# Kernel tuning notes

Measured on AMD Instinct MI355X. Metric: run time of the kernel, lower is better.

## Reference

```python
import jax, jax.numpy as jnp
import numpy as np

NUM_HEADS = 8
PW_GROUPS = 3 * NUM_HEADS  # grouped 1x1 conv groups


def _conv(x, w, groups):
    # x: [B, Cin, H, W], w: [Cout, Cin/groups, kh, kw]
    return jax.lax.conv_general_dilated(
        x, w, window_strides=(1, 1), padding='SAME',
        feature_group_count=groups,
        dimension_numbers=('NCHW', 'OIHW', 'NCHW'))


def setup_inputs() -> dict:
    key = jax.random.key(0)
    ks = jax.random.split(key, 12)
    dim, N, B = 512, 4096, 2
    C = dim // 2  # 256
    s = 0.02
    return {
        'x': jax.random.normal(ks[0], (B, N, dim), jnp.float32),
        'w_reduce': jax.random.normal(ks[1], (dim, C), jnp.float32) * s,
        'w_qkv': jax.random.normal(ks[2], (C, 3 * C), jnp.float32) * s,
        'dw0': jax.random.normal(ks[3], (3 * C, 1, 3, 3), jnp.float32) * s,
        'pw0': jax.random.normal(ks[4], (3 * C, 3 * C // PW_GROUPS, 1, 1), jnp.float32) * s,
        'dw1': jax.random.normal(ks[5], (3 * C, 1, 5, 5), jnp.float32) * s,
        'pw1': jax.random.normal(ks[6], (3 * C, 3 * C // PW_GROUPS, 1, 1), jnp.float32) * s,
        'dw2': jax.random.normal(ks[7], (3 * C, 1, 7, 7), jnp.float32) * s,
        'pw2': jax.random.normal(ks[8], (3 * C, 3 * C // PW_GROUPS, 1, 1), jnp.float32) * s,
        'w_reduce2': jax.random.normal(ks[9], (6 * dim, 3 * C), jnp.float32) * s,
        'w_proj': jax.random.normal(ks[10], (C, dim), jnp.float32) * s,
        'b_proj': jax.random.normal(ks[11], (dim,), jnp.float32) * s,
    }


def reference(x, w_reduce, w_qkv, dw0, pw0, dw1, pw1, dw2, pw2,
              w_reduce2, w_proj, b_proj):
    B, N, dim = x.shape
    Hn = NUM_HEADS
    x = x @ w_reduce                       # [B, N, C]
    C = x.shape[-1]
    hd = C // Hn
    scale = hd ** -0.5
    Hs = int(np.sqrt(N))                   # spatial side

    qkv = x @ w_qkv                        # [B, N, 3C]
    qkv_img = qkv.transpose(0, 2, 1).reshape(B, 3 * C, Hs, Hs)

    branches = [qkv_img]
    for dw, pw in ((dw0, pw0), (dw1, pw1), (dw2, pw2)):
        y = _conv(qkv_img, dw, groups=3 * C)      # depthwise
        y = _conv(y, pw, groups=PW_GROUPS)        # grouped 1x1
        branches.append(y)
    cat = jnp.concatenate(branches, axis=1)       # [B, 12C, Hs, Hs]
    cat = cat.reshape(B, 12 * C, N).transpose(0, 2, 1)  # [B, N, 6*dim]
    msq = cat @ w_reduce2                          # [B, N, 3C]

    qkv = msq.reshape(B, N, 3, Hn, hd).transpose(2, 0, 3, 1, 4)  # [3,B,H,N,hd]
    q, k, v = qkv[0], qkv[1], qkv[2]

    # chunked attention: 2 chunks of N//2 tokens, attention within each chunk
    Nc = N // 2
    qc = q.reshape(B, Hn, 2, Nc, hd)
    kc = k.reshape(B, Hn, 2, Nc, hd)
    vc = v.reshape(B, Hn, 2, Nc, hd)
    attn = jnp.einsum('bhcqd,bhckd->bhcqk', qc, kc) * scale
    attn = jax.nn.softmax(attn, axis=-1)
    out = jnp.einsum('bhcqk,bhckd->bhcqd', attn, vc)  # [B,H,2,Nc,hd]
    out = out.transpose(0, 2, 3, 1, 4).reshape(B, N, C)
    return out @ w_proj + b_proj                  # [B, N, dim]
```

## Files before the change

kernel.cpp:

```cpp
#include <hip/hip_runtime.h>
#include <hip/hip_bf16.h>

typedef __bf16 bf16x8 __attribute__((ext_vector_type(8)));
typedef __bf16 bf16x4v __attribute__((ext_vector_type(4)));
typedef float f32x4 __attribute__((ext_vector_type(4)));
typedef unsigned int u32x4 __attribute__((ext_vector_type(4)));

using bf16 = __hip_bfloat16;

__global__ __launch_bounds__(256) void k_cvt_bf16(const float* __restrict__ in,
                                                  bf16* __restrict__ out) {
  const int i = (blockIdx.x * 256 + threadIdx.x) * 4;
  float4 v = *reinterpret_cast<const float4*>(in + i);
  out[i + 0] = __float2bfloat16(v.x);
  out[i + 1] = __float2bfloat16(v.y);
  out[i + 2] = __float2bfloat16(v.z);
  out[i + 3] = __float2bfloat16(v.w);
}

__global__ __launch_bounds__(256) void k_transpose_bf16(const float* __restrict__ w,
                                                        bf16* __restrict__ wt,
                                                        int K, int N) {
  __shared__ float t[32][33];
  const int k0 = blockIdx.x * 32, n0 = blockIdx.y * 32;
  const int tx = threadIdx.x & 31, ty = threadIdx.x >> 5;
#pragma unroll
  for (int i = 0; i < 32; i += 8)
    t[ty + i][tx] = w[(size_t)(k0 + ty + i) * N + n0 + tx];
  __syncthreads();
#pragma unroll
  for (int i = 0; i < 32; i += 8)
    wt[(size_t)(n0 + ty + i) * K + k0 + tx] = __float2bfloat16(t[tx][ty + i]);
}

__global__ __launch_bounds__(256) void k_transpose2d(const bf16* __restrict__ in,
                                                     bf16* __restrict__ out,
                                                     int R, int C) {
  __shared__ unsigned short tl[64][65];
  const int c0 = blockIdx.x * 64, r0 = blockIdx.y * 64;
  const size_t zb = (size_t)blockIdx.z * R * C;
  const int tx = threadIdx.x & 63, ty = threadIdx.x >> 6;
  const unsigned short* ip = (const unsigned short*)in + zb;
  unsigned short* op = (unsigned short*)out + zb;
#pragma unroll
  for (int i = 0; i < 64; i += 4)
    tl[ty + i][tx] = ip[(size_t)(r0 + ty + i) * C + c0 + tx];
  __syncthreads();
#pragma unroll
  for (int i = 0; i < 64; i += 4)
    op[(size_t)(c0 + ty + i) * R + r0 + tx] = tl[tx][ty + i];
}

__global__ __launch_bounds__(256) void k_gemm_bt(
    const bf16* __restrict__ A0, const bf16* __restrict__ A1,
    const bf16* __restrict__ A2, const bf16* __restrict__ A3,
    const bf16* __restrict__ Bt, bf16* __restrict__ Cb,
    float* __restrict__ Cf, const float* __restrict__ bias,
    int N, int K, int srcK, int split_bk) {
  __shared__ __align__(16) bf16 As[2][128 * 64];
  __shared__ __align__(16) bf16 Bs[2][128 * 64];
  const int tid = threadIdx.x;
  const int lane = tid & 63;
  const int wv = tid >> 6;
  const size_t M0 = (size_t)blockIdx.x * 128;
  const int N0 = blockIdx.y * 128;
  const int wr = (wv >> 1) * 64, wc = (wv & 1) * 64;
  const int fr = lane & 15, fo = (lane >> 4) * 8;
  const int lrow = lane >> 3, lcol = (lane & 7) << 3;
  f32x4 acc[4][4] = {};

  auto stage = [&](int kt, int buf) {
    const int s = kt / split_bk;
    const bf16* __restrict__ Ak = (s == 0) ? A0 : (s == 1) ? A1 : (s == 2) ? A2 : A3;
    const size_t aofs = (size_t)(kt - s * split_bk) * 64;
    const size_t bofs = (size_t)kt * 64;
#pragma unroll
    for (int ld = 0; ld < 4; ++ld) {
      const int row = wv * 32 + ld * 8 + lrow;
      const bf16* ga = Ak + (M0 + row) * (size_t)srcK + aofs + lcol;
      __builtin_amdgcn_global_load_lds(
          (const __attribute__((address_space(1))) unsigned int*)ga,
          (__attribute__((address_space(3))) unsigned int*)(As[buf] + (wv * 32 + ld * 8) * 64),
          16, 0, 0);
      const bf16* gb = Bt + (size_t)(N0 + row) * K + bofs + lcol;
      __builtin_amdgcn_global_load_lds(
          (const __attribute__((address_space(1))) unsigned int*)gb,
          (__attribute__((address_space(3))) unsigned int*)(Bs[buf] + (wv * 32 + ld * 8) * 64),
          16, 0, 0);
    }
  };

  const int nsteps = K >> 6;
  stage(0, 0);
  __syncthreads();
  int cur = 0;
  for (int kt = 0; kt < nsteps; ++kt) {
    if (kt + 1 < nsteps) stage(kt + 1, cur ^ 1);
#pragma unroll
    for (int kk = 0; kk < 64; kk += 32) {
      bf16x8 a[4], b[4];
#pragma unroll
      for (int m = 0; m < 4; ++m)
        a[m] = *reinterpret_cast<const bf16x8*>(As[cur] + (wr + m * 16 + fr) * 64 + kk + fo);
#pragma unroll
      for (int n = 0; n < 4; ++n)
        b[n] = *reinterpret_cast<const bf16x8*>(Bs[cur] + (wc + n * 16 + fr) * 64 + kk + fo);
#pragma unroll
      for (int m = 0; m < 4; ++m)
#pragma unroll
        for (int n = 0; n < 4; ++n)
          acc[m][n] = __builtin_amdgcn_mfma_f32_16x16x32_bf16(a[m], b[n], acc[m][n], 0, 0, 0);
    }
    __syncthreads();
    cur ^= 1;
  }

  const int rb = (lane >> 4) * 4;
#pragma unroll
  for (int m = 0; m < 4; ++m) {
#pragma unroll
    for (int n = 0; n < 4; ++n) {
      const size_t row = M0 + wr + m * 16 + rb;
      const int col = N0 + wc + n * 16 + fr;
      if (Cb != nullptr) {
#pragma unroll
        for (int r = 0; r < 4; ++r)
          Cb[(row + r) * N + col] = __float2bfloat16(acc[m][n][r]);
      } else {
        const float bb = bias[col];
#pragma unroll
        for (int r = 0; r < 4; ++r)
          Cf[(row + r) * N + col] = acc[m][n][r] + bb;
      }
    }
  }
}

template <int KS>
__global__ __launch_bounds__(256) void k_dwconv_img(const bf16* __restrict__ in,
                                                    const float* __restrict__ w,
                                                    bf16* __restrict__ out) {
  constexpr int P = KS / 2;
  constexpr int ROWS = 64 + 2 * P;
  constexpr int PITCH = 80;
  constexpr int NCHUNK = ROWS * PITCH * 2 / 16;
  __shared__ __align__(16) bf16 pl[ROWS * PITCH];
  const int t = threadIdx.x;
  const int c = blockIdx.x, b = blockIdx.y;
  const bf16* __restrict__ ip = in + ((size_t)b * 768 + c) * 4096;
  bf16* __restrict__ op = out + ((size_t)b * 768 + c) * 4096;

  u32x4* pl4 = reinterpret_cast<u32x4*>(pl);
  for (int i = t; i < NCHUNK; i += 256) pl4[i] = u32x4{0, 0, 0, 0};
  __syncthreads();
  for (int q = t; q < 512; q += 256) {
    const int px0 = q * 8;
    const int y = px0 >> 6, x = px0 & 63;
    u32x4 v = *reinterpret_cast<const u32x4*>(ip + px0);
    *reinterpret_cast<u32x4*>(&pl[(y + P) * PITCH + 8 + x]) = v;
  }
  __syncthreads();

  float wk[KS * KS];
#pragma unroll
  for (int i = 0; i < KS * KS; ++i) wk[i] = w[c * KS * KS + i];

  const int x = t & 63;
  const int y0 = (t >> 6) * 16;
  float win[KS][KS];
#pragma unroll
  for (int r = 0; r < 2 * P; ++r)
#pragma unroll
    for (int kx = 0; kx < KS; ++kx)
      win[r % KS][kx] = __bfloat162float(pl[(y0 + r) * PITCH + 8 + x - P + kx]);
#pragma unroll
  for (int yy = 0; yy < 16; ++yy) {
    constexpr int twoP = 2 * P;
#pragma unroll
    for (int kx = 0; kx < KS; ++kx)
      win[(yy + twoP) % KS][kx] =
          __bfloat162float(pl[(y0 + yy + twoP) * PITCH + 8 + x - P + kx]);
    float acc = 0.f;
#pragma unroll
    for (int ky = 0; ky < KS; ++ky)
#pragma unroll
      for (int kx = 0; kx < KS; ++kx)
        acc += win[(yy + ky) % KS][kx] * wk[ky * KS + kx];
    op[(y0 + yy) * 64 + x] = __float2bfloat16(acc);
  }
}

__global__ __launch_bounds__(256) void k_pwconv_img(const bf16* __restrict__ in,
                                                    const float* __restrict__ w,
                                                    bf16* __restrict__ out) {
  const int co0 = blockIdx.x * 4;
  const int g = co0 >> 5;
  const int b = blockIdx.z;
  const int px = blockIdx.y * 2048 + threadIdx.x * 8;
  const bf16* __restrict__ ip = in + ((size_t)b * 768 + g * 32) * 4096 + px;
  float acc[4][8] = {};
#pragma unroll
  for (int ci = 0; ci < 32; ++ci) {
    const bf16x8 v = *reinterpret_cast<const bf16x8*>(ip + (size_t)ci * 4096);
    float fv[8];
#pragma unroll
    for (int j = 0; j < 8; ++j) fv[j] = (float)v[j];
#pragma unroll
    for (int q = 0; q < 4; ++q) {
      const float wq = w[(co0 + q) * 32 + ci];
#pragma unroll
      for (int j = 0; j < 8; ++j) acc[q][j] += wq * fv[j];
    }
  }
#pragma unroll
  for (int q = 0; q < 4; ++q) {
    bf16x8 o;
#pragma unroll
    for (int j = 0; j < 8; ++j) o[j] = (__bf16)acc[q][j];
    *reinterpret_cast<bf16x8*>(out + ((size_t)b * 768 + co0 + q) * 4096 + px) = o;
  }
}

__global__ __launch_bounds__(256) void k_attn(const bf16* __restrict__ msq,
                                              bf16* __restrict__ out) {
  const int qt = blockIdx.x;
  const int combo = blockIdx.y;
  const int b = combo >> 4;
  const int h = (combo >> 1) & 7;
  const int ck = combo & 1;
  const int tid = threadIdx.x, lane = tid & 63, wv = tid >> 6;
  const int fr = lane & 15, hi = lane >> 4, fo = hi * 8;
  const size_t base = (size_t)b * 4096 * 768;
  const int n0 = ck * 2048 + qt * 128;

  __shared__ __align__(16) bf16 Kl[2][64][40];
  __shared__ __align__(16) bf16 Vt[2][32][72];
  __shared__ __align__(16) bf16 Pl[4][2][16][72];

  const float scale = 0.17677669529663687f;
  bf16x8 qf[2];
#pragma unroll
  for (int t = 0; t < 2; ++t) {
    const int qrow = n0 + t * 64 + wv * 16 + fr;
    const bf16x8 v =
        *reinterpret_cast<const bf16x8*>(msq + base + (size_t)qrow * 768 + h * 32 + fo);
#pragma unroll
    for (int j = 0; j < 8; ++j) qf[t][j] = (__bf16)((float)v[j] * scale);
  }

  f32x4 oacc[2][2] = {};
  float mrun[2] = {-1e30f, -1e30f};
  float lrun[2] = {0.f, 0.f};
  const int sr = tid >> 2, sdc = (tid & 3) << 3;

  u32x4 kr, vr;
  auto gload = [&](int kt) {
    const size_t rbase = base + (size_t)(ck * 2048 + kt * 64 + sr) * 768 + h * 32;
    kr = *reinterpret_cast<const u32x4*>(msq + rbase + 256 + sdc);
    vr = *reinterpret_cast<const u32x4*>(msq + rbase + 512 + sdc);
  };
  auto lwrite = [&](int buf) {
    *reinterpret_cast<u32x4*>(&Kl[buf][sr][sdc]) = kr;
    const bf16* vp = reinterpret_cast<const bf16*>(&vr);
#pragma unroll
    for (int j = 0; j < 8; ++j) Vt[buf][sdc + j][sr] = vp[j];
  };

  gload(0);
  lwrite(0);
  int cur = 0;
  for (int kt = 0; kt < 32; ++kt) {
    __syncthreads();
    if (kt + 1 < 32) gload(kt + 1);

    bf16x8 kf[4];
#pragma unroll
    for (int j = 0; j < 4; ++j)
      kf[j] = *reinterpret_cast<const bf16x8*>(&Kl[cur][j * 16 + fr][fo]);

#pragma unroll
    for (int t = 0; t < 2; ++t) {
      f32x4 sacc[4];
#pragma unroll
      for (int j = 0; j < 4; ++j) {
        const f32x4 z = {0.f, 0.f, 0.f, 0.f};
        sacc[j] = __builtin_amdgcn_mfma_f32_16x16x32_bf16(kf[j], qf[t], z, 0, 0, 0);
      }
      float mx = -1e30f;
#pragma unroll
      for (int j = 0; j < 4; ++j)
#pragma unroll
        for (int r = 0; r < 4; ++r) mx = fmaxf(mx, sacc[j][r]);
      mx = fmaxf(mx, __shfl_xor(mx, 16));
      mx = fmaxf(mx, __shfl_xor(mx, 32));
      const float mnew = fmaxf(mrun[t], mx);
      const float corr = __expf(mrun[t] - mnew);
      mrun[t] = mnew;
      float sm = 0.f;
#pragma unroll
      for (int j = 0; j < 4; ++j) {
        bf16x4v pk;
#pragma unroll
        for (int r = 0; r < 4; ++r) {
          const float pz = __expf(sacc[j][r] - mnew);
          sm += pz;
          pk[r] = (__bf16)pz;
        }
        *reinterpret_cast<bf16x4v*>(&Pl[wv][t][fr][j * 16 + hi * 4]) = pk;
      }
      sm += __shfl_xor(sm, 16);
      sm += __shfl_xor(sm, 32);
      lrun[t] = lrun[t] * corr + sm;
#pragma unroll
      for (int r = 0; r < 4; ++r) {
        const float cf = __shfl(corr, hi * 4 + r);
        oacc[t][0][r] *= cf;
        oacc[t][1][r] *= cf;
      }
    }

#pragma unroll
    for (int t = 0; t < 2; ++t)
#pragma unroll
      for (int kk = 0; kk < 2; ++kk) {
        const bf16x8 pa = *reinterpret_cast<const bf16x8*>(&Pl[wv][t][fr][kk * 32 + fo]);
#pragma unroll
        for (int nb = 0; nb < 2; ++nb) {
          const bf16x8 vb =
              *reinterpret_cast<const bf16x8*>(&Vt[cur][nb * 16 + fr][kk * 32 + fo]);
          oacc[t][nb] = __builtin_amdgcn_mfma_f32_16x16x32_bf16(pa, vb, oacc[t][nb], 0, 0, 0);
        }
      }

    if (kt + 1 < 32) lwrite(cur ^ 1);
    cur ^= 1;
  }

#pragma unroll
  for (int t = 0; t < 2; ++t)
#pragma unroll
    for (int r = 0; r < 4; ++r) {
      const float lf = __shfl(lrun[t], hi * 4 + r);
      const float inv = 1.f / lf;
      const int row = n0 + t * 64 + wv * 16 + hi * 4 + r;
#pragma unroll
      for (int nb = 0; nb < 2; ++nb)
        out[((size_t)b * 4096 + row) * 256 + h * 32 + nb * 16 + fr] =
            __float2bfloat16(oacc[t][nb][r] * inv);
    }
}

extern "C" void kernel_launch(void* const* d_in, const int* in_sizes, int n_in,
                              void* d_out, int out_size, void* d_ws, size_t ws_size,
                              hipStream_t stream) {
  (void)in_sizes; (void)n_in; (void)out_size; (void)ws_size;
  const float* x    = (const float*)d_in[0];
  const float* wrd  = (const float*)d_in[1];
  const float* wqkv = (const float*)d_in[2];
  const float* dw0  = (const float*)d_in[3];
  const float* pw0  = (const float*)d_in[4];
  const float* dw1  = (const float*)d_in[5];
  const float* pw1  = (const float*)d_in[6];
  const float* dw2  = (const float*)d_in[7];
  const float* pw2  = (const float*)d_in[8];
  const float* wrd2 = (const float*)d_in[9];
  const float* wprj = (const float*)d_in[10];
  const float* bprj = (const float*)d_in[11];
  float* out = (float*)d_out;

  char* p = (char*)d_ws;
  auto nxt = [&](size_t bytes) {
    char* r = p;
    p += (bytes + 255) & ~(size_t)255;
    return (bf16*)r;
  };
  bf16* xb   = nxt(8192ull * 512 * 2);
  bf16* xr   = nxt(8192ull * 256 * 2);
  bf16* qkvT = xb;
  bf16* wrT  = nxt(256ull * 512 * 2);
  bf16* wqT  = nxt(768ull * 256 * 2);
  bf16* wr2T = nxt(768ull * 3072 * 2);
  bf16* wpT  = nxt(512ull * 256 * 2);
  bf16* qkv  = nxt(8192ull * 768 * 2);
  bf16* dtmp = nxt(8192ull * 768 * 2);
  bf16* y0   = nxt(8192ull * 768 * 2);
  bf16* y1   = nxt(8192ull * 768 * 2);
  bf16* y2   = nxt(8192ull * 768 * 2);
  bf16* msq  = nxt(8192ull * 768 * 2);
  bf16* pwT  = msq;
  bf16* ao   = nxt(8192ull * 256 * 2);

  k_cvt_bf16<<<(8192 * 512 / 4) / 256, 256, 0, stream>>>(x, xb);
  k_transpose_bf16<<<dim3(512 / 32, 256 / 32), 256, 0, stream>>>(wrd, wrT, 512, 256);
  k_transpose_bf16<<<dim3(256 / 32, 768 / 32), 256, 0, stream>>>(wqkv, wqT, 256, 768);
  k_transpose_bf16<<<dim3(3072 / 32, 768 / 32), 256, 0, stream>>>(wrd2, wr2T, 3072, 768);
  k_transpose_bf16<<<dim3(256 / 32, 512 / 32), 256, 0, stream>>>(wprj, wpT, 256, 512);

  k_gemm_bt<<<dim3(64, 2), 256, 0, stream>>>(xb, xb, xb, xb, wrT, xr, nullptr, nullptr,
                                             256, 512, 512, 1 << 20);
  k_gemm_bt<<<dim3(64, 6), 256, 0, stream>>>(xr, xr, xr, xr, wqT, qkv, nullptr, nullptr,
                                             768, 256, 256, 1 << 20);

  k_transpose2d<<<dim3(12, 64, 2), 256, 0, stream>>>(qkv, qkvT, 4096, 768);

  k_dwconv_img<3><<<dim3(768, 2), 256, 0, stream>>>(qkvT, dw0, dtmp);
  k_pwconv_img<<<dim3(192, 2, 2), 256, 0, stream>>>(dtmp, pw0, pwT);
  k_transpose2d<<<dim3(64, 12, 2), 256, 0, stream>>>(pwT, y0, 768, 4096);

  k_dwconv_img<5><<<dim3(768, 2), 256, 0, stream>>>(qkvT, dw1, dtmp);
  k_pwconv_img<<<dim3(192, 2, 2), 256, 0, stream>>>(dtmp, pw1, pwT);
  k_transpose2d<<<dim3(64, 12, 2), 256, 0, stream>>>(pwT, y1, 768, 4096);

  k_dwconv_img<7><<<dim3(768, 2), 256, 0, stream>>>(qkvT, dw2, dtmp);
  k_pwconv_img<<<dim3(192, 2, 2), 256, 0, stream>>>(dtmp, pw2, pwT);
  k_transpose2d<<<dim3(64, 12, 2), 256, 0, stream>>>(pwT, y2, 768, 4096);

  k_gemm_bt<<<dim3(64, 6), 256, 0, stream>>>(qkv, y0, y1, y2, wr2T, msq, nullptr, nullptr,
                                             768, 3072, 768, 12);

  k_attn<<<dim3(16, 32), 256, 0, stream>>>(msq, ao);

  k_gemm_bt<<<dim3(64, 4), 256, 0, stream>>>(ao, ao, ao, ao, wpT, nullptr, out, bprj,
                                             512, 256, 256, 1 << 20);
}
```

Measured before the change: 375.2 us.

## Fold linear weights algebraically, drop pwconv kernels, retile attention with lazy rescale

Precomputes w_reduce@w_qkv into one fused weight so two GEMMs become one. Folds each grouped 1x1 pointwise conv into the corresponding rows of w_reduce2, which removes three pwconv kernels and their intermediate traffic. The attention kernel now handles 64 queries per block with twice as many blocks, skips the online-softmax rescale unless the running max grows by more than a threshold, and XOR-swizzles the V tile in shared memory to cut bank conflicts. Weight folding rounds the combined products to bf16 and changes accumulation order, so numerics shift slightly.

```diff
diff --git a/kernel.cpp b/kernel.cpp
--- a/kernel.cpp
+++ b/kernel.cpp
@@ -31,6 +31,55 @@
 #pragma unroll
   for (int i = 0; i < 32; i += 8)
     wt[(size_t)(n0 + ty + i) * K + k0 + tx] = __float2bfloat16(t[tx][ty + i]);
+}
+
+__global__ __launch_bounds__(256) void k_fuse_w12(const float* __restrict__ wrd,
+                                                  const float* __restrict__ wqkv,
+                                                  bf16* __restrict__ w12T) {
+  const int n = blockIdx.x * 64 + (threadIdx.x & 63);
+  const int k0 = blockIdx.y * 64 + (threadIdx.x >> 6) * 16;
+  float acc[16] = {};
+  for (int j = 0; j < 256; ++j) {
+    const float wq = wqkv[(size_t)j * 768 + n];
+#pragma unroll
+    for (int e = 0; e < 16; ++e) acc[e] += wrd[(size_t)(k0 + e) * 256 + j] * wq;
+  }
+  bf16x8 o0, o1;
+#pragma unroll
+  for (int e = 0; e < 8; ++e) { o0[e] = (__bf16)acc[e]; o1[e] = (__bf16)acc[8 + e]; }
+  *reinterpret_cast<bf16x8*>(w12T + (size_t)n * 512 + k0) = o0;
+  *reinterpret_cast<bf16x8*>(w12T + (size_t)n * 512 + k0 + 8) = o1;
+}
+
+__global__ __launch_bounds__(256) void k_fuse_pw(const float* __restrict__ pw0,
+                                                 const float* __restrict__ pw1,
+                                                 const float* __restrict__ pw2,
+                                                 const float* __restrict__ w2,
+                                                 bf16* __restrict__ wr2T) {
+  const int g = blockIdx.x;
+  const int n0 = blockIdx.y * 64;
+  const int i = blockIdx.z;
+  const float* __restrict__ pw = (i == 0) ? pw0 : (i == 1) ? pw1 : pw2;
+  __shared__ float pwL[32][36];
+  {
+    const int q = threadIdx.x >> 3, c4 = (threadIdx.x & 7) * 4;
+    float4 v = *reinterpret_cast<const float4*>(pw + (size_t)(g * 32 + q) * 32 + c4);
+    *reinterpret_cast<float4*>(&pwL[q][c4]) = v;
+  }
+  __syncthreads();
+  const int n = n0 + (threadIdx.x & 63);
+  const int ch = threadIdx.x >> 6;
+  const int kbase = 768 * (i + 1) + g * 32;
+  float acc[8] = {};
+  for (int q = 0; q < 32; ++q) {
+    const float w2v = w2[(size_t)(kbase + q) * 768 + n];
+#pragma unroll
+    for (int e = 0; e < 8; ++e) acc[e] += pwL[q][ch * 8 + e] * w2v;
+  }
+  bf16x8 o;
+#pragma unroll
+  for (int e = 0; e < 8; ++e) o[e] = (__bf16)acc[e];
+  *reinterpret_cast<bf16x8*>(wr2T + (size_t)n * 3072 + kbase + ch * 8) = o;
 }
 
 __global__ __launch_bounds__(256) void k_transpose2d(const bf16* __restrict__ in,
@@ -190,37 +239,6 @@
   }
 }
 
-__global__ __launch_bounds__(256) void k_pwconv_img(const bf16* __restrict__ in,
-                                                    const float* __restrict__ w,
-                                                    bf16* __restrict__ out) {
-  const int co0 = blockIdx.x * 4;
-  const int g = co0 >> 5;
-  const int b = blockIdx.z;
-  const int px = blockIdx.y * 2048 + threadIdx.x * 8;
-  const bf16* __restrict__ ip = in + ((size_t)b * 768 + g * 32) * 4096 + px;
-  float acc[4][8] = {};
-#pragma unroll
-  for (int ci = 0; ci < 32; ++ci) {
-    const bf16x8 v = *reinterpret_cast<const bf16x8*>(ip + (size_t)ci * 4096);
-    float fv[8];
-#pragma unroll
-    for (int j = 0; j < 8; ++j) fv[j] = (float)v[j];
-#pragma unroll
-    for (int q = 0; q < 4; ++q) {
-      const float wq = w[(co0 + q) * 32 + ci];
-#pragma unroll
-      for (int j = 0; j < 8; ++j) acc[q][j] += wq * fv[j];
-    }
-  }
-#pragma unroll
-  for (int q = 0; q < 4; ++q) {
-    bf16x8 o;
-#pragma unroll
-    for (int j = 0; j < 8; ++j) o[j] = (__bf16)acc[q][j];
-    *reinterpret_cast<bf16x8*>(out + ((size_t)b * 768 + co0 + q) * 4096 + px) = o;
-  }
-}
-
 __global__ __launch_bounds__(256) void k_attn(const bf16* __restrict__ msq,
                                               bf16* __restrict__ out) {
   const int qt = blockIdx.x;
@@ -231,27 +249,26 @@
   const int tid = threadIdx.x, lane = tid & 63, wv = tid >> 6;
   const int fr = lane & 15, hi = lane >> 4, fo = hi * 8;
   const size_t base = (size_t)b * 4096 * 768;
-  const int n0 = ck * 2048 + qt * 128;
+  const int n0 = ck * 2048 + qt * 64;
 
   __shared__ __align__(16) bf16 Kl[2][64][40];
   __shared__ __align__(16) bf16 Vt[2][32][72];
-  __shared__ __align__(16) bf16 Pl[4][2][16][72];
+  __shared__ __align__(16) bf16 Pl[4][16][72];
 
   const float scale = 0.17677669529663687f;
-  bf16x8 qf[2];
-#pragma unroll
-  for (int t = 0; t < 2; ++t) {
-    const int qrow = n0 + t * 64 + wv * 16 + fr;
+  bf16x8 qf;
+  {
+    const int qrow = n0 + wv * 16 + fr;
     const bf16x8 v =
         *reinterpret_cast<const bf16x8*>(msq + base + (size_t)qrow * 768 + h * 32 + fo);
 #pragma unroll
-    for (int j = 0; j < 8; ++j) qf[t][j] = (__bf16)((float)v[j] * scale);
-  }
-
-  f32x4 oacc[2][2] = {};
-  float mrun[2] = {-1e30f, -1e30f};
-  float lrun[2] = {0.f, 0.f};
+    for (int j = 0; j < 8; ++j) qf[j] = (__bf16)((float)v[j] * scale);
+  }
+
+  f32x4 oacc[2] = {};
+  float mrun = 0.f, lrun = 0.f;
   const int sr = tid >> 2, sdc = (tid & 3) << 3;
+  const int vswz = (tid & 3) << 4;
 
   u32x4 kr, vr;
   auto gload = [&](int kt) {
@@ -263,7 +280,7 @@
     *reinterpret_cast<u32x4*>(&Kl[buf][sr][sdc]) = kr;
     const bf16* vp = reinterpret_cast<const bf16*>(&vr);
 #pragma unroll
-    for (int j = 0; j < 8; ++j) Vt[buf][sdc + j][sr] = vp[j];
+    for (int j = 0; j < 8; ++j) Vt[buf][sdc + j][sr ^ vswz] = vp[j];
   };
 
   gload(0);
@@ -273,81 +290,74 @@
     __syncthreads();
     if (kt + 1 < 32) gload(kt + 1);
 
-    bf16x8 kf[4];
+    f32x4 sacc[4];
+#pragma unroll
+    for (int j = 0; j < 4; ++j) {
+      const bf16x8 kf = *reinterpret_cast<const bf16x8*>(&Kl[cur][j * 16 + fr][fo]);
+      const f32x4 z = {0.f, 0.f, 0.f, 0.f};
+      sacc[j] = __builtin_amdgcn_mfma_f32_16x16x32_bf16(kf, qf, z, 0, 0, 0);
+    }
+    float mx = -1e30f;
 #pragma unroll
     for (int j = 0; j < 4; ++j)
-      kf[j] = *reinterpret_cast<const bf16x8*>(&Kl[cur][j * 16 + fr][fo]);
-
-#pragma unroll
-    for (int t = 0; t < 2; ++t) {
-      f32x4 sacc[4];
-#pragma unroll
-      for (int j = 0; j < 4; ++j) {
-        const f32x4 z = {0.f, 0.f, 0.f, 0.f};
-        sacc[j] = __builtin_amdgcn_mfma_f32_16x16x32_bf16(kf[j], qf[t], z, 0, 0, 0);
-      }
-      float mx = -1e30f;
-#pragma unroll
-      for (int j = 0; j < 4; ++j)
-#pragma unroll
-        for (int r = 0; r < 4; ++r) mx = fmaxf(mx, sacc[j][r]);
-      mx = fmaxf(mx, __shfl_xor(mx, 16));
-      mx = fmaxf(mx, __shfl_xor(mx, 32));
-      const float mnew = fmaxf(mrun[t], mx);
-      const float corr = __expf(mrun[t] - mnew);
-      mrun[t] = mnew;
-      float sm = 0.f;
-#pragma unroll
-      for (int j = 0; j < 4; ++j) {
-        bf16x4v pk;
-#pragma unroll
-        for (int r = 0; r < 4; ++r) {
-          const float pz = __expf(sacc[j][r] - mnew);
-          sm += pz;
-          pk[r] = (__bf16)pz;
-        }
-        *reinterpret_cast<bf16x4v*>(&Pl[wv][t][fr][j * 16 + hi * 4]) = pk;
-      }
-      sm += __shfl_xor(sm, 16);
-      sm += __shfl_xor(sm, 32);
-      lrun[t] = lrun[t] * corr + sm;
+#pragma unroll
+      for (int r = 0; r < 4; ++r) mx = fmaxf(mx, sacc[j][r]);
+    mx = fmaxf(mx, __shfl_xor(mx, 16));
+    mx = fmaxf(mx, __shfl_xor(mx, 32));
+    if (!__all(mx <= mrun + 8.f)) {
+      const float mnew = fmaxf(mrun, mx);
+      const float corr = __expf(mrun - mnew);
+      mrun = mnew;
+      lrun *= corr;
 #pragma unroll
       for (int r = 0; r < 4; ++r) {
         const float cf = __shfl(corr, hi * 4 + r);
-        oacc[t][0][r] *= cf;
-        oacc[t][1][r] *= cf;
+        oacc[0][r] *= cf;
+        oacc[1][r] *= cf;
       }
     }
-
-#pragma unroll
-    for (int t = 0; t < 2; ++t)
-#pragma unroll
-      for (int kk = 0; kk < 2; ++kk) {
-        const bf16x8 pa = *reinterpret_cast<const bf16x8*>(&Pl[wv][t][fr][kk * 32 + fo]);
-#pragma unroll
-        for (int nb = 0; nb < 2; ++nb) {
-          const bf16x8 vb =
-              *reinterpret_cast<const bf16x8*>(&Vt[cur][nb * 16 + fr][kk * 32 + fo]);
-          oacc[t][nb] = __builtin_amdgcn_mfma_f32_16x16x32_bf16(pa, vb, oacc[t][nb], 0, 0, 0);
-        }
+    float sm = 0.f;
+#pragma unroll
+    for (int j = 0; j < 4; ++j) {
+      bf16x4v pk;
+#pragma unroll
+      for (int r = 0; r < 4; ++r) {
+        const float pz = __expf(sacc[j][r] - mrun);
+        sm += pz;
+        pk[r] = (__bf16)pz;
       }
+      *reinterpret_cast<bf16x4v*>(&Pl[wv][fr][j * 16 + hi * 4]) = pk;
+    }
+    sm += __shfl_xor(sm, 16);
+    sm += __shfl_xor(sm, 32);
+    lrun += sm;
+
+#pragma unroll
+    for (int kk = 0; kk < 2; ++kk) {
+      const bf16x8 pa = *reinterpret_cast<const bf16x8*>(&Pl[wv][fr][kk * 32 + fo]);
+#pragma unroll
+      for (int nb = 0; nb < 2; ++nb) {
+        const int d = nb * 16 + fr;
+        const int colb = (kk * 32 + fo) ^ (((d >> 3) & 3) << 4);
+        const bf16x8 vb = *reinterpret_cast<const bf16x8*>(&Vt[cur][d][colb]);
+        oacc[nb] = __builtin_amdgcn_mfma_f32_16x16x32_bf16(pa, vb, oacc[nb], 0, 0, 0);
+      }
+    }
 
     if (kt + 1 < 32) lwrite(cur ^ 1);
     cur ^= 1;
   }
 
 #pragma unroll
-  for (int t = 0; t < 2; ++t)
-#pragma unroll
-    for (int r = 0; r < 4; ++r) {
-      const float lf = __shfl(lrun[t], hi * 4 + r);
-      const float inv = 1.f / lf;
-      const int row = n0 + t * 64 + wv * 16 + hi * 4 + r;
-#pragma unroll
-      for (int nb = 0; nb < 2; ++nb)
-        out[((size_t)b * 4096 + row) * 256 + h * 32 + nb * 16 + fr] =
-            __float2bfloat16(oacc[t][nb][r] * inv);
-    }
+  for (int r = 0; r < 4; ++r) {
+    const float lf = __shfl(lrun, hi * 4 + r);
+    const float inv = 1.f / lf;
+    const int row = n0 + wv * 16 + hi * 4 + r;
+#pragma unroll
+    for (int nb = 0; nb < 2; ++nb)
+      out[((size_t)b * 4096 + row) * 256 + h * 32 + nb * 16 + fr] =
+          __float2bfloat16(oacc[nb][r] * inv);
+  }
 }
 
 extern "C" void kernel_launch(void* const* d_in, const int* in_sizes, int n_in,
@@ -375,10 +385,7 @@
     return (bf16*)r;
   };
   bf16* xb   = nxt(8192ull * 512 * 2);
-  bf16* xr   = nxt(8192ull * 256 * 2);
-  bf16* qkvT = xb;
-  bf16* wrT  = nxt(256ull * 512 * 2);
-  bf16* wqT  = nxt(768ull * 256 * 2);
+  bf16* w12T = nxt(768ull * 512 * 2);
   bf16* wr2T = nxt(768ull * 3072 * 2);
   bf16* wpT  = nxt(512ull * 256 * 2);
   bf16* qkv  = nxt(8192ull * 768 * 2);
@@ -387,38 +394,31 @@
   bf16* y1   = nxt(8192ull * 768 * 2);
   bf16* y2   = nxt(8192ull * 768 * 2);
   bf16* msq  = nxt(8192ull * 768 * 2);
-  bf16* pwT  = msq;
+  bf16* qkvT = msq;
   bf16* ao   = nxt(8192ull * 256 * 2);
 
   k_cvt_bf16<<<(8192 * 512 / 4) / 256, 256, 0, stream>>>(x, xb);
-  k_transpose_bf16<<<dim3(512 / 32, 256 / 32), 256, 0, stream>>>(wrd, wrT, 512, 256);
-  k_transpose_bf16<<<dim3(256 / 32, 768 / 32), 256, 0, stream>>>(wqkv, wqT, 256, 768);
-  k_transpose_bf16<<<dim3(3072 / 32, 768 / 32), 256, 0, stream>>>(wrd2, wr2T, 3072, 768);
+  k_fuse_w12<<<dim3(12, 8), 256, 0, stream>>>(wrd, wqkv, w12T);
+  k_transpose_bf16<<<dim3(24, 24), 256, 0, stream>>>(wrd2, wr2T, 3072, 768);
+  k_fuse_pw<<<dim3(24, 12, 3), 256, 0, stream>>>(pw0, pw1, pw2, wrd2, wr2T);
   k_transpose_bf16<<<dim3(256 / 32, 512 / 32), 256, 0, stream>>>(wprj, wpT, 256, 512);
 
-  k_gemm_bt<<<dim3(64, 2), 256, 0, stream>>>(xb, xb, xb, xb, wrT, xr, nullptr, nullptr,
-                                             256, 512, 512, 1 << 20);
-  k_gemm_bt<<<dim3(64, 6), 256, 0, stream>>>(xr, xr, xr, xr, wqT, qkv, nullptr, nullptr,
-                                             768, 256, 256, 1 << 20);
+  k_gemm_bt<<<dim3(64, 6), 256, 0, stream>>>(xb, xb, xb, xb, w12T, qkv, nullptr, nullptr,
+                                             768, 512, 512, 1 << 20);
 
   k_transpose2d<<<dim3(12, 64, 2), 256, 0, stream>>>(qkv, qkvT, 4096, 768);
 
   k_dwconv_img<3><<<dim3(768, 2), 256, 0, stream>>>(qkvT, dw0, dtmp);
-  k_pwconv_img<<<dim3(192, 2, 2), 256, 0, stream>>>(dtmp, pw0, pwT);
-  k_transpose2d<<<dim3(64, 12, 2), 256, 0, stream>>>(pwT, y0, 768, 4096);
-
+  k_transpose2d<<<dim3(64, 12, 2), 256, 0, stream>>>(dtmp, y0, 768, 4096);
   k_dwconv_img<5><<<dim3(768, 2), 256, 0, stream>>>(qkvT, dw1, dtmp);
-  k_pwconv_img<<<dim3(192, 2, 2), 256, 0, stream>>>(dtmp, pw1, pwT);
-  k_transpose2d<<<dim3(64, 12, 2), 256, 0, stream>>>(pwT, y1, 768, 4096);
-
+  k_transpose2d<<<dim3(64, 12, 2), 256, 0, stream>>>(dtmp, y1, 768, 4096);
   k_dwconv_img<7><<<dim3(768, 2), 256, 0, stream>>>(qkvT, dw2, dtmp);
-  k_pwconv_img<<<dim3(192, 2, 2), 256, 0, stream>>>(dtmp, pw2, pwT);
-  k_transpose2d<<<dim3(64, 12, 2), 256, 0, stream>>>(pwT, y2, 768, 4096);
+  k_transpose2d<<<dim3(64, 12, 2), 256, 0, stream>>>(dtmp, y2, 768, 4096);
 
   k_gemm_bt<<<dim3(64, 6), 256, 0, stream>>>(qkv, y0, y1, y2, wr2T, msq, nullptr, nullptr,
                                              768, 3072, 768, 12);
 
-  k_attn<<<dim3(16, 32), 256, 0, stream>>>(msq, ao);
+  k_attn<<<dim3(32, 32), 256, 0, stream>>>(msq, ao);
 
   k_gemm_bt<<<dim3(64, 4), 256, 0, stream>>>(ao, ao, ao, ao, wpT, nullptr, out, bprj,
                                              512, 256, 256, 1 << 20);
```

Measured after the change: 373.4 us. No clear change (-0.5%).
